# Performance work log

Hardware: AMD Instinct MI355X
Metric: run time of the kernel (lower is better)

Reference implementation:

```python
import jax, jax.numpy as jnp
import numpy as np

B, S, D = 1, 4096, 2048
M = 4                  # compression rate
NC = S // M            # compressed slots
TOPK = 512
NH, C = 16, 64         # query heads, head dim
DC = 512               # query compression dim
NG, DG = 4, 512        # output projection groups, intermediate dim
CI, NHI = 64, 4        # indexer head dim, indexer heads
ROPE = 32              # partial rope dims (last ROPE of C)
EPS = 1e-6
NEG = -1e30


def _ln(x, w, b):
    mu = x.mean(-1, keepdims=True)
    var = ((x - mu) ** 2).mean(-1, keepdims=True)
    return (x - mu) * jax.lax.rsqrt(var + EPS) * w + b


def _rope(q, pos):
    # partial RoPE on the last ROPE dims of q [B,S,NH,C]; keys are NOT rotated (faithful)
    x_part, x_rope = q[..., :C - ROPE], q[..., C - ROPE:]
    x0, x1 = x_rope[..., 0::2], x_rope[..., 1::2]
    inv = 1.0 / (10000.0 ** (jnp.arange(0, ROPE, 2, dtype=jnp.float32) / ROPE))
    ang = pos[:, None].astype(jnp.float32) * inv[None]           # [S, ROPE/2]
    cos = jnp.cos(ang)[None, :, None, :]
    sin = jnp.sin(ang)[None, :, None, :]
    r = x0 * cos - x1 * sin
    i = x0 * sin + x1 * cos
    rot = jnp.stack([r, i], -1).reshape(x_rope.shape)
    return jnp.concatenate([x_part, rot], -1)


def reference(x, w_kv_a, w_kv_b, w_z_a, w_z_b, b_a, b_b, w_dq, w_iuq, w_w, w_k,
              w_uq, o_down, o_up, kvn_w, kvn_b, qn_w, qn_b, sink_logits):
    pos = jnp.arange(S)
    # ---- token-level compressor: windowed (2m-wide, m-stride) per-channel softmax ----
    c_a = (x @ w_kv_a).reshape(B, NC, M, C)
    c_b = (x @ w_kv_b).reshape(B, NC, M, C)
    z_a = (x @ w_z_a).reshape(B, NC, M, C)
    z_b = (x @ w_z_b).reshape(B, NC, M, C)
    prev_z = jnp.concatenate([jnp.full((B, 1, M, C), NEG, x.dtype), z_b[:, :-1]], 1)
    prev_c = jnp.concatenate([jnp.zeros((B, 1, M, C), x.dtype), c_b[:, :-1]], 1)
    logits = jnp.concatenate([prev_z + b_b, z_a + b_a], 2)        # [B,NC,2M,C]
    wts = jax.nn.softmax(logits, axis=2)
    compressed = (wts * jnp.concatenate([prev_c, c_a], 2)).sum(2)  # [B,NC,C]
    # ---- lightning indexer: relu multi-head scores + causal mask + top-k ----
    c_q = x @ w_dq                                                 # [B,S,DC]
    q_i = (c_q @ w_iuq).reshape(B, S, NHI, CI)
    hw = x @ w_w                                                   # [B,S,NHI]
    k_orig = x.reshape(B, NC, M, D).mean(2)
    k_proj = k_orig @ w_k                                          # [B,NC,CI]
    dot = jnp.einsum('bshc,bkc->bskh', q_i, k_proj)
    iscores = (jax.nn.relu(dot) * hw[:, :, None, :]).sum(-1)       # [B,S,NC]
    imask = jnp.arange(NC)[None, None, :] < pos[None, :, None]     # NC//S + 1 == 1
    iscores = jnp.where(imask, iscores, -jnp.inf)
    _, top_idx = jax.lax.top_k(iscores, TOPK)                      # [B,S,K]
    # ---- sparse attention over gathered compressed KV ----
    q = (c_q @ w_uq).reshape(B, S, NH, C)
    kc = _ln(compressed, kvn_w, kvn_b)
    q = _rope(_ln(q, qn_w, qn_b), pos)
    k_sel = kc[jnp.arange(B)[:, None, None], top_idx]              # [B,S,K,C]
    scores = jnp.einsum('bshc,bskc->bhsk', q, k_sel) / jnp.sqrt(jnp.float32(C))
    cmask = pos[None, None, :, None] < (top_idx[:, None, :, :] * M)
    scores = jnp.where(cmask, scores, -jnp.inf)
    e = jnp.exp(scores)
    denom = e.sum(-1, keepdims=True) + jnp.exp(sink_logits)[None, :, None, None]
    attn = e / denom                                               # sink-augmented softmax
    out = jnp.einsum('bhsk,bskc->bshc', attn, k_sel).reshape(B, S, NH * C)
    g = jnp.einsum('bsgd,gde->bsge', out.reshape(B, S, NG, (NH * C) // NG), o_down)
    return g.reshape(B, S, NG * DG) @ o_up


def setup_inputs() -> dict:
    key = jax.random.key(0)
    ks = jax.random.split(key, 20)
    lin = lambda k, fi, fo: jax.random.normal(k, (fi, fo), jnp.float32) / np.sqrt(fi)
    return {
        'x': jax.random.normal(ks[0], (B, S, D), jnp.float32),
        'w_kv_a': lin(ks[1], D, C), 'w_kv_b': lin(ks[2], D, C),
        'w_z_a': lin(ks[3], D, C), 'w_z_b': lin(ks[4], D, C),
        'b_a': 0.02 * jax.random.normal(ks[5], (M, C), jnp.float32),
        'b_b': 0.02 * jax.random.normal(ks[6], (M, C), jnp.float32),
        'w_dq': lin(ks[7], D, DC),
        'w_iuq': lin(ks[8], DC, CI * NHI),
        'w_w': lin(ks[9], D, NHI),
        'w_k': lin(ks[10], D, CI),
        'w_uq': lin(ks[11], DC, NH * C),
        'o_down': jax.random.normal(ks[12], (NG, (NH * C) // NG, DG), jnp.float32) / np.sqrt((NH * C) // NG),
        'o_up': lin(ks[13], NG * DG, D),
        'kvn_w': 1.0 + 0.02 * jax.random.normal(ks[14], (C,), jnp.float32),
        'kvn_b': 0.02 * jax.random.normal(ks[15], (C,), jnp.float32),
        'qn_w': 1.0 + 0.02 * jax.random.normal(ks[16], (C,), jnp.float32),
        'qn_b': 0.02 * jax.random.normal(ks[17], (C,), jnp.float32),
        'sink_logits': 0.02 * jax.random.normal(ks[18], (NH,), jnp.float32),
    }
```

## Files before the change

### kernel.cpp

```cpp
#include <hip/hip_runtime.h>
#include <math.h>

#define S_   4096
#define D_   2048
#define M_   4
#define NC_  1024
#define TOPK_ 512
#define NH_  16
#define C_   64
#define DC_  512
#define NG_  4
#define DG_  512
#define CI_  64
#define NHI_ 4
#define ROPE_ 32
#define EPS_ 1e-6f

typedef __attribute__((ext_vector_type(8))) short short8;
typedef __attribute__((ext_vector_type(4))) short short4v;
typedef __attribute__((ext_vector_type(4))) float floatx4;

__device__ inline unsigned short f2bf(float f) {
  unsigned u = __float_as_uint(f);
  u += 0x7fff + ((u >> 16) & 1);
// ... 390 lines not shown
  float4 a = *(const float4*)&P[i];
  for (int s = 1; s < z; ++s) {
    float4 b = *(const float4*)&P[(size_t)s * n + i];
    a.x += b.x; a.y += b.y; a.z += b.z; a.w += b.w;
  }
  *(float4*)&C[i] = a;
}

__global__ void reduce_cast_split(const float* __restrict__ P, unsigned short* __restrict__ hi,
                                  unsigned short* __restrict__ lo, int n, int z) {
  int i = (blockIdx.x * 256 + threadIdx.x) * 4;
  if (i >= n) return;
  float4 a = *(const float4*)&P[i];
  for (int s = 1; s < z; ++s) {
    float4 b = *(const float4*)&P[(size_t)s * n + i];
    a.x += b.x; a.y += b.y; a.z += b.z; a.w += b.w;
  }
  ushort4 h = make_ushort4(f2bf(a.x), f2bf(a.y), f2bf(a.z), f2bf(a.w));
  ushort4 l = make_ushort4(f2bf(a.x - bf2f(h.x)), f2bf(a.y - bf2f(h.y)),
                           f2bf(a.z - bf2f(h.z)), f2bf(a.w - bf2f(h.w)));
  *(ushort4*)&hi[i] = h;
  *(ushort4*)&lo[i] = l;
}

__global__ __launch_bounds__(256) void iscores_mfma(
    const unsigned short* __restrict__ Ah, const unsigned short* __restrict__ Al,
    const unsigned short* __restrict__ Bh, const unsigned short* __restrict__ Bl,
    const float* __restrict__ hw, float* __restrict__ isc) {
  int bm = blockIdx.y * 128, bn = blockIdx.x * 128;
  if (bn > (bm >> 2) + 30) return;
  __shared__ unsigned short Ash[128 * 32];
  __shared__ unsigned short Asl[128 * 32];
  __shared__ unsigned short Bsh[128 * 32];
  __shared__ unsigned short Bsl[128 * 32];
  int tid = threadIdx.x;
  int lane = tid & 63, wid = tid >> 6;
  int wm = (wid >> 1) * 64, wn = (wid & 1) * 64;
  int qd = lane >> 4, m16 = lane & 15;

  floatx4 acc[4][4];
#pragma unroll
  for (int i = 0; i < 4; ++i)
#pragma unroll
    for (int j = 0; j < 4; ++j) acc[i][j] = (floatx4){0.f, 0.f, 0.f, 0.f};

#pragma unroll
  for (int k0 = 0; k0 < 64; k0 += 32) {
#pragma unroll
    for (int i = 0; i < 2; ++i) {
      int idx = tid + 256 * i;
      int r = idx >> 2, s = idx & 3;
      int g = s ^ ((r >> 1) & 3);
      size_t aoff = (size_t)(bm + r) * 64 + k0 + g * 8;
      size_t boff = (size_t)(bn + r) * 64 + k0 + g * 8;
      GLD16(Ah + aoff, &Ash[idx * 8]);
      GLD16(Al + aoff, &Asl[idx * 8]);
      GLD16(Bh + boff, &Bsh[idx * 8]);
      GLD16(Bl + boff, &Bsl[idx * 8]);
    }
    __syncthreads();
    short8 afh[4], afl[4], bfh[4], bfl[4];
#pragma unroll
    for (int mi = 0; mi < 4; ++mi) {
      int r = wm + mi * 16 + m16;
      int slot = qd ^ ((r >> 1) & 3);
      afh[mi] = *(const short8*)&Ash[r * 32 + slot * 8];
      afl[mi] = *(const short8*)&Asl[r * 32 + slot * 8];
    }
#pragma unroll
    for (int ni = 0; ni < 4; ++ni) {
      int r = wn + ni * 16 + m16;
      int slot = qd ^ ((r >> 1) & 3);
      bfh[ni] = *(const short8*)&Bsh[r * 32 + slot * 8];
      bfl[ni] = *(const short8*)&Bsl[r * 32 + slot * 8];
    }
#pragma unroll
    for (int mi = 0; mi < 4; ++mi)
#pragma unroll
      for (int ni = 0; ni < 4; ++ni) {
        acc[mi][ni] = __builtin_amdgcn_mfma_f32_16x16x32_bf16(afh[mi], bfh[ni], acc[mi][ni], 0, 0, 0);
        acc[mi][ni] = __builtin_amdgcn_mfma_f32_16x16x32_bf16(afh[mi], bfl[ni], acc[mi][ni], 0, 0, 0);
        acc[mi][ni] = __builtin_amdgcn_mfma_f32_16x16x32_bf16(afl[mi], bfh[ni], acc[mi][ni], 0, 0, 0);
      }
    __syncthreads();
  }
#pragma unroll
  for (int mi = 0; mi < 4; ++mi) {
    int tok = ((bm + wm + mi * 16) >> 2) + qd;
    float4 hwv = *(const float4*)&hw[tok * 4];
#pragma unroll
    for (int ni = 0; ni < 4; ++ni) {
      floatx4 a = acc[mi][ni];
      float v = fmaxf(a[0], 0.f) * hwv.x + fmaxf(a[1], 0.f) * hwv.y +
                fmaxf(a[2], 0.f) * hwv.z + fmaxf(a[3], 0.f) * hwv.w;
      int col = bn + wn + ni * 16 + m16;
      isc[(size_t)tok * NC_ + col] = (col < tok) ? v : -__builtin_inff();
    }
  }
}

#define BM 64
#define BN 64
#define BK 16
#define KSL_ 16
#define KSLICE_ 128
__global__ __launch_bounds__(256) void gemm_f32_splitk(
    const float* __restrict__ A, const float* __restrict__ B,
    float* __restrict__ P, int lda, int ldb) {
  __shared__ float As[BK][BM + 4];
  __shared__ float Bs[BK][BN + 4];
  int tid = threadIdx.x;
  int bm = blockIdx.y * BM;
  int kbase = blockIdx.x * KSLICE_;
  int tr = tid >> 4;
  int tc = tid & 15;
  float acc[4][4] = {{0.f}};
  for (int k0 = kbase; k0 < kbase + KSLICE_; k0 += BK) {
    int ac = tid & 15;
    int ar0 = tid >> 4;
#pragma unroll
    for (int i = 0; i < 4; ++i) {
      int r = ar0 + 16 * i;
      As[ac][r] = A[(size_t)(bm + r) * lda + k0 + ac];
    }
    int bc = tid & 63;
    int br0 = tid >> 6;
#pragma unroll
    for (int i = 0; i < 4; ++i) {
      int r = br0 + 4 * i;
      Bs[r][bc] = B[(size_t)(k0 + r) * ldb + bc];
    }
    __syncthreads();
#pragma unroll
    for (int kk = 0; kk < BK; ++kk) {
      float4 av = *(const float4*)&As[kk][tr * 4];
      float4 bv = *(const float4*)&Bs[kk][tc * 4];
      float a[4] = {av.x, av.y, av.z, av.w};
      float b[4] = {bv.x, bv.y, bv.z, bv.w};
#pragma unroll
      for (int i = 0; i < 4; ++i)
#pragma unroll
        for (int j = 0; j < 4; ++j) acc[i][j] += a[i] * b[j];
    }
    __syncthreads();
  }
  float* Pb = P + (size_t)blockIdx.x * (NC_ * CI_);
#pragma unroll
  for (int i = 0; i < 4; ++i) {
    float4 v = make_float4(acc[i][0], acc[i][1], acc[i][2], acc[i][3]);
    *(float4*)&Pb[(size_t)(bm + tr * 4 + i) * CI_ + tc * 4] = v;
  }
}

__global__ void reduce_splitk(const float* __restrict__ P, float* __restrict__ C) {
  int i = blockIdx.x * 256 + threadIdx.x;
  if (i >= NC_ * CI_) return;
  float a = 0.f;
#pragma unroll
  for (int s = 0; s < KSL_; ++s) a += P[(size_t)s * (NC_ * CI_) + i];
  C[i] = a;
}

__global__ void cast_bf16(const float* __restrict__ in, unsigned short* __restrict__ out, int n) {
  int i = (blockIdx.x * 256 + threadIdx.x) * 4;
  if (i >= n) return;
  float4 v = *(const float4*)&in[i];
  ushort4 o = make_ushort4(f2bf(v.x), f2bf(v.y), f2bf(v.z), f2bf(v.w));
  *(ushort4*)&out[i] = o;
}

__global__ void cast_split(const float* __restrict__ in, unsigned short* __restrict__ hi,
                           unsigned short* __restrict__ lo, int n) {
  int i = (blockIdx.x * 256 + threadIdx.x) * 4;
  if (i >= n) return;
  float4 v = *(const float4*)&in[i];
  ushort4 h = make_ushort4(f2bf(v.x), f2bf(v.y), f2bf(v.z), f2bf(v.w));
  ushort4 l = make_ushort4(f2bf(v.x - bf2f(h.x)), f2bf(v.y - bf2f(h.y)),
                           f2bf(v.z - bf2f(h.z)), f2bf(v.w - bf2f(h.w)));
  *(ushort4*)&hi[i] = h;
  *(ushort4*)&lo[i] = l;
}

__device__ inline float wave_sum64(float v) {
#pragma unroll
  for (int off = 32; off > 0; off >>= 1) v += __shfl_xor(v, off, 64);
  return v;
}

__global__ __launch_bounds__(512) void cast_split_hw_mean(
    const float* __restrict__ x, unsigned short* __restrict__ hi,
    unsigned short* __restrict__ lo, const float* __restrict__ ww,
    float* __restrict__ hw, float* __restrict__ ko) {
  int j = blockIdx.x, tid = threadIdx.x;
  int d0 = tid * 4;
  const float* wr = ww + d0 * 4;
  float4 v[4];
  float a[4][4];
#pragma unroll
  for (int m = 0; m < 4; ++m) {
    size_t i = (size_t)(j * 4 + m) * D_ + d0;
    v[m] = *(const float4*)&x[i];
    ushort4 h = make_ushort4(f2bf(v[m].x), f2bf(v[m].y), f2bf(v[m].z), f2bf(v[m].w));
    ushort4 l = make_ushort4(f2bf(v[m].x - bf2f(h.x)), f2bf(v[m].y - bf2f(h.y)),
                             f2bf(v[m].z - bf2f(h.z)), f2bf(v[m].w - bf2f(h.w)));
    *(ushort4*)&hi[i] = h;
    *(ushort4*)&lo[i] = l;
    a[m][0] = v[m].x * wr[0] + v[m].y * wr[4] + v[m].z * wr[8]  + v[m].w * wr[12];
    a[m][1] = v[m].x * wr[1] + v[m].y * wr[5] + v[m].z * wr[9]  + v[m].w * wr[13];
    a[m][2] = v[m].x * wr[2] + v[m].y * wr[6] + v[m].z * wr[10] + v[m].w * wr[14];
    a[m][3] = v[m].x * wr[3] + v[m].y * wr[7] + v[m].z * wr[11] + v[m].w * wr[15];
  }
  float4 s4;
  s4.x = 0.25f * (v[0].x + v[1].x + v[2].x + v[3].x);
  s4.y = 0.25f * (v[0].y + v[1].y + v[2].y + v[3].y);
  s4.z = 0.25f * (v[0].z + v[1].z + v[2].z + v[3].z);
  s4.w = 0.25f * (v[0].w + v[1].w + v[2].w + v[3].w);
  *(float4*)&ko[(size_t)j * D_ + d0] = s4;
#pragma unroll
  for (int m = 0; m < 4; ++m)
#pragma unroll
    for (int h2 = 0; h2 < 4; ++h2) a[m][h2] = wave_sum64(a[m][h2]);
  __shared__ float red[8][16];
  int wid = tid >> 6, lane = tid & 63;
  if (lane == 0) {
#pragma unroll
    for (int m = 0; m < 4; ++m)
#pragma unroll
      for (int h2 = 0; h2 < 4; ++h2) red[wid][m * 4 + h2] = a[m][h2];
  }
  __syncthreads();
  if (tid < 16) {
    float acc = 0.f;
#pragma unroll
    for (int w2 = 0; w2 < 8; ++w2) acc += red[w2][tid];
    hw[(size_t)(j * 4 + (tid >> 2)) * 4 + (tid & 3)] = acc;
  }
}

__global__ __launch_bounds__(256) void transpose_cast(
    const float* __restrict__ in, unsigned short* __restrict__ out, int K, int N,
    long long inz, long long outz) {
  in += (size_t)blockIdx.z * inz;
  out += (size_t)blockIdx.z * outz;
  __shared__ float t[32][33];
  int k0 = blockIdx.x * 32, n0 = blockIdx.y * 32;
  int tx = threadIdx.x & 31, ty = threadIdx.x >> 5;
#pragma unroll
  for (int i = 0; i < 4; ++i)
    t[ty * 4 + i][tx] = in[(size_t)(k0 + ty * 4 + i) * N + n0 + tx];
  __syncthreads();
#pragma unroll
  for (int i = 0; i < 4; ++i)
    out[(size_t)(n0 + ty * 4 + i) * K + k0 + tx] = f2bf(t[tx][ty * 4 + i]);
}

__global__ __launch_bounds__(256) void transpose_cast_split(
    const float* __restrict__ in, unsigned short* __restrict__ outh,
    unsigned short* __restrict__ outl, int K, int N) {
  __shared__ float t[32][33];
  int k0 = blockIdx.x * 32, n0 = blockIdx.y * 32;
  int tx = threadIdx.x & 31, ty = threadIdx.x >> 5;
#pragma unroll
  for (int i = 0; i < 4; ++i)
    t[ty * 4 + i][tx] = in[(size_t)(k0 + ty * 4 + i) * N + n0 + tx];
  __syncthreads();
#pragma unroll
  for (int i = 0; i < 4; ++i) {
    float v = t[tx][ty * 4 + i];
    unsigned short h = f2bf(v);
    outh[(size_t)(n0 + ty * 4 + i) * K + k0 + tx] = h;
    outl[(size_t)(n0 + ty * 4 + i) * K + k0 + tx] = f2bf(v - bf2f(h));
  }
}

__global__ void gate_kernel(const float* __restrict__ c4,
                            const float* __restrict__ ba, const float* __restrict__ bb,
                            float* __restrict__ comp) {
  int i = blockIdx.x * 256 + threadIdx.x;
  if (i >= NC_ * C_) return;
  int j = i >> 6, c = i & 63;
  float lg[8], vv[8];
#pragma unroll
  for (int m = 0; m < 4; ++m) {
    if (j == 0) {
      lg[m] = -1e30f + bb[m * C_ + c];
      vv[m] = 0.f;
    } else {
      int row = (j - 1) * 4 + m;
      lg[m] = c4[(size_t)row * 256 + 192 + c] + bb[m * C_ + c];
      vv[m] = c4[(size_t)row * 256 + 64 + c];
    }
    int row2 = j * 4 + m;
    lg[4 + m] = c4[(size_t)row2 * 256 + 128 + c] + ba[m * C_ + c];
    vv[4 + m] = c4[(size_t)row2 * 256 + 0 + c];
  }
  float mx = lg[0];
#pragma unroll
  for (int t = 1; t < 8; ++t) mx = fmaxf(mx, lg[t]);
  float se = 0.f, acc = 0.f;
#pragma unroll
  for (int t = 0; t < 8; ++t) {
    float e = expf(lg[t] - mx);
    se += e;
    acc += e * vv[t];
  }
  comp[i] = acc / se;
}

__global__ void ln_kc_kernel(const float* __restrict__ in, const float* __restrict__ w,
                             const float* __restrict__ b, unsigned short* __restrict__ kcb,
                             unsigned short* __restrict__ kcbT) {
  int row = blockIdx.x * 4 + (threadIdx.x >> 6);
  int c = threadIdx.x & 63;
  float v = in[(size_t)row * C_ + c];
  float mu = wave_sum64(v) * (1.f / 64.f);
  float d = v - mu;
  float var = wave_sum64(d * d) * (1.f / 64.f);
  float y = d * (1.f / sqrtf(var + EPS_)) * w[c] + b[c];
  unsigned short h = f2bf(y);
  kcb[(size_t)row * C_ + c] = h;
  kcbT[(size_t)c * NC_ + row] = h;
}

__global__ void rope_table_kernel(float* __restrict__ rt) {
  int i = blockIdx.x * 256 + threadIdx.x;
  if (i >= S_ * 16) return;
  int s = i >> 4, p = i & 15;
  float inv = powf(10000.f, -(2.f * (float)p) / (float)ROPE_);
  float ang = (float)s * inv;
  rt[i * 2] = cosf(ang);
  rt[i * 2 + 1] = sinf(ang);
}

__global__ void ln_rope_q_kernel(const float* __restrict__ quq, const float* __restrict__ w,
                                 const float* __restrict__ b, const float* __restrict__ rt,
                                 unsigned short* __restrict__ qb) {
  int row = blockIdx.x * 4 + (threadIdx.x >> 6);
  int s = row >> 4;
  int c = threadIdx.x & 63;
  float v = quq[(size_t)row * C_ + c];
  float mu = wave_sum64(v) * (1.f / 64.f);
  float d = v - mu;
  float var = wave_sum64(d * d) * (1.f / 64.f);
  float y = d * (1.f / sqrtf(var + EPS_)) * w[c] + b[c];
  float outv;
  float partner = __shfl_xor(y, 1, 64);
  if (c < C_ - ROPE_) {
    outv = y;
  } else {
    int p = (c - (C_ - ROPE_)) >> 1;
    float cs = rt[(s * 16 + p) * 2];
    float sn = rt[(s * 16 + p) * 2 + 1];
    if ((c & 1) == 0)
      outv = y * cs - partner * sn;
    else
      outv = partner * sn + y * cs;
  }
  qb[(size_t)row * C_ + c] = f2bf(outv * 0.125f);
}

#define MINF_ 0x007FFFFFu
__global__ __launch_bounds__(256) void topk_select_kernel(
    const float* __restrict__ isc, unsigned* __restrict__ sel) {
  __shared__ unsigned mv[NC_];
  __shared__ unsigned bins[256];
  __shared__ unsigned wsum[4];
  __shared__ unsigned sB, sR;
  __shared__ unsigned selw[32];
  int s = blockIdx.x;
  int tid = threadIdx.x;
  int w = tid >> 6, lane = tid & 63;
  if (tid < 32) selw[tid] = 0u;
  for (int i = tid; i < NC_; i += 256) {
    if (i < s) {
      unsigned u = __float_as_uint(isc[(size_t)s * NC_ + i]);
      mv[i] = (u & 0x80000000u) ? ~u : (u | 0x80000000u);
    } else {
      mv[i] = MINF_;
    }
  }
  __syncthreads();
  unsigned K_rem = TOPK_;
  unsigned prefix = 0u;
  for (int lvl = 0; lvl < 4; ++lvl) {
    int shift = 24 - 8 * lvl;
    unsigned pm = (lvl == 0) ? 0u : (0xFFFFFFFFu << (32 - 8 * lvl));
    bins[tid] = 0u;
    __syncthreads();
    for (int i = tid; i < NC_; i += 256) {
      unsigned m = mv[i];
      if ((m & pm) == prefix) atomicAdd(&bins[(m >> shift) & 0xFFu], 1u);
    }
    __syncthreads();
    unsigned v = bins[tid];
    unsigned p = v;
#pragma unroll
    for (int off = 1; off < 64; off <<= 1) {
      unsigned n = __shfl_up(p, (unsigned)off, 64);
      if (lane >= off) p += n;
    }
    if (lane == 63) wsum[w] = p;
    __syncthreads();
    unsigned T = 0, woff = 0;
#pragma unroll
    for (int i = 0; i < 4; ++i) {
      unsigned x_ = wsum[i];
      T += x_;
      if (i < w) woff += x_;
    }
    p += woff;
    unsigned gt = T - p;
    if (gt < K_rem && K_rem <= gt + v) { sB = (unsigned)tid; sR = K_rem - gt; }
    __syncthreads();
    prefix |= (sB << shift);
    K_rem = sR;
  }
  unsigned vstar = prefix;
  unsigned eq = 0;
#pragma unroll
  for (int j = 0; j < 4; ++j) eq += (mv[4 * tid + j] == vstar);
  unsigned rp = eq;
#pragma unroll
  for (int off = 1; off < 64; off <<= 1) {
    unsigned n = __shfl_up(rp, (unsigned)off, 64);
    if (lane >= off) rp += n;
  }
  if (lane == 63) wsum[w] = rp;
  __syncthreads();
  unsigned woff2 = 0;
#pragma unroll
  for (int i = 0; i < 4; ++i)
    if (i < w) woff2 += wsum[i];
  unsigned rank0 = rp + woff2 - eq;
  unsigned local = 0, bits = 0;
#pragma unroll
  for (int j = 0; j < 4; ++j) {
    unsigned m = mv[4 * tid + j];
    bool sb = (m > vstar) || (m == vstar && (rank0 + local) < K_rem);
    local += (m == vstar);
    if (sb) bits |= (1u << ((4 * tid + j) & 31));
  }
  if (bits) atomicOr(&selw[tid >> 3], bits);
  __syncthreads();
  if (tid < 32) sel[(size_t)s * 32 + tid] = selw[tid];
}

#define TS_ 8
__global__ __launch_bounds__(256) void attn_mfma_kernel(
    const unsigned short* __restrict__ qb, const unsigned short* __restrict__ kcb,
    const unsigned short* __restrict__ kcbT, const unsigned* __restrict__ sel,
    const float* __restrict__ sink, unsigned short* __restrict__ out) {
  __shared__ unsigned short p_s[128 * 72];
  __shared__ unsigned selw[TS_][32];
  int tid = threadIdx.x;
  int s0 = blockIdx.x * TS_;
  int lane = tid & 63, w = tid >> 6;
  int qd = lane >> 4, m16 = lane & 15;

  selw[tid >> 5][tid & 31] = sel[(size_t)(s0 + (tid >> 5)) * 32 + (tid & 31)];

  short8 qf[2][2];
#pragma unroll
  for (int tk = 0; tk < 2; ++tk)
#pragma unroll
    for (int ks = 0; ks < 2; ++ks)
      qf[tk][ks] = *(const short8*)&qb[(size_t)(s0 + 2 * w + tk) * 1024 + m16 * 64 + ks * 32 + qd * 8];

  floatx4 of[2][4];
#pragma unroll
  for (int i = 0; i < 2; ++i)
#pragma unroll
    for (int j = 0; j < 4; ++j) of[i][j] = (floatx4){0.f, 0.f, 0.f, 0.f};
  float dsum[2] = {0.f, 0.f};

  int ub = max(511, s0 + TS_ - 2);
  int ct_start = max(0, (s0 + 4) >> 8);
  int ct_end = min(16, (ub >> 6) + 1);

  for (int ct = ct_start; ct < ct_end; ++ct) {
    int c0 = ct * 64;
#pragma unroll
    for (int mc = 0; mc < 4; ++mc) {
      short8 a0 = *(const short8*)&kcb[(size_t)(c0 + mc * 16 + m16) * 64 + qd * 8];
      short8 a1 = *(const short8*)&kcb[(size_t)(c0 + mc * 16 + m16) * 64 + 32 + qd * 8];
#pragma unroll
      for (int nt = 0; nt < 2; ++nt) {
        floatx4 sc = (floatx4){0.f, 0.f, 0.f, 0.f};
        sc = __builtin_amdgcn_mfma_f32_16x16x32_bf16(a0, qf[nt][0], sc, 0, 0, 0);
        sc = __builtin_amdgcn_mfma_f32_16x16x32_bf16(a1, qf[nt][1], sc, 0, 0, 0);
        int tokL = 2 * w + nt;
        int sG = s0 + tokL;
        short4v pv;
#pragma unroll
        for (int rg = 0; rg < 4; ++rg) {
          int cG = c0 + mc * 16 + qd * 4 + rg;
          bool ok = (((selw[tokL][cG >> 5] >> (cG & 31)) & 1u) != 0u) && (sG < cG * 4);
          float e = ok ? __expf(sc[rg]) : 0.f;
          dsum[nt] += e;
          pv[rg] = (short)f2bf(e);
        }
        *(short4v*)&p_s[(tokL * 16 + m16) * 72 + mc * 16 + qd * 4] = pv;
      }
    }
#pragma unroll
    for (int ks = 0; ks < 2; ++ks) {
      short8 pa0 = *(const short8*)&p_s[((2 * w + 0) * 16 + m16) * 72 + ks * 32 + qd * 8];
      short8 pa1 = *(const short8*)&p_s[((2 * w + 1) * 16 + m16) * 72 + ks * 32 + qd * 8];
#pragma unroll
      for (int nt = 0; nt < 4; ++nt) {
        short8 bv = *(const short8*)&kcbT[(size_t)(nt * 16 + m16) * NC_ + c0 + ks * 32 + qd * 8];
        of[0][nt] = __builtin_amdgcn_mfma_f32_16x16x32_bf16(pa0, bv, of[0][nt], 0, 0, 0);
        of[1][nt] = __builtin_amdgcn_mfma_f32_16x16x32_bf16(pa1, bv, of[1][nt], 0, 0, 0);
      }
    }
  }
#pragma unroll
  for (int nt = 0; nt < 2; ++nt) {
    dsum[nt] += __shfl_xor(dsum[nt], 16, 64);
    dsum[nt] += __shfl_xor(dsum[nt], 32, 64);
  }
#pragma unroll
  for (int tk = 0; tk < 2; ++tk)
#pragma unroll
    for (int nt = 0; nt < 4; ++nt) {
      floatx4 o = of[tk][nt];
#pragma unroll
      for (int rg = 0; rg < 4; ++rg) {
        int head = qd * 4 + rg;
        float dn = __shfl(dsum[tk], head, 64) + __expf(sink[head]);
        out[(size_t)(s0 + 2 * w + tk) * 1024 + head * 64 + nt * 16 + m16] = f2bf(o[rg] / dn);
      }
    }
}

#define OFF_QUQ    0u
#define OFF_Q      4194304u
#define OFF_XH     8388608u
#define OFF_XL     12582912u
#define OFF_PART   16777216u
#define OFF_KO     18874368u
#define OFF_C4     20971520u
#define OFF_CQF    22020096u
#define OFF_RT     23134208u
#define OFF_WTB    24117248u
#define OFF_CQH    25165824u
#define OFF_CQL    26214400u
#define OFF_WPACKT 27262976u
#define OFF_WDQTH  27525120u
#define OFF_WDQTL  28049408u
#define OFF_WIUQTH 28573696u
#define OFF_WIUQTL 28639232u
#define OFF_WUQT   28704768u
#define OFF_ODB    28966912u
#define OFF_OUPT   29229056u
#define OFF_HW     31326208u
#define OFF_COMP   31342592u
#define OFF_KC     31408128u
#define OFF_KPR    31473664u

extern "C" void kernel_launch(void* const* d_in, const int* in_sizes, int n_in,
                              void* d_out, int out_size, void* d_ws, size_t ws_size,
                              hipStream_t stream) {
  const float* x      = (const float*)d_in[0];
  const float* w_kv_a = (const float*)d_in[1];
  const float* w_kv_b = (const float*)d_in[2];
  const float* w_z_a  = (const float*)d_in[3];
  const float* w_z_b  = (const float*)d_in[4];
  const float* b_a    = (const float*)d_in[5];
  const float* b_b    = (const float*)d_in[6];
  const float* w_dq   = (const float*)d_in[7];
  const float* w_iuq  = (const float*)d_in[8];
  const float* w_w    = (const float*)d_in[9];
  const float* w_k    = (const float*)d_in[10];
  const float* w_uq   = (const float*)d_in[11];
  const float* o_down = (const float*)d_in[12];
  const float* o_up   = (const float*)d_in[13];
  const float* kvn_w  = (const float*)d_in[14];
  const float* kvn_b  = (const float*)d_in[15];
  const float* qn_w   = (const float*)d_in[16];
  const float* qn_b   = (const float*)d_in[17];
  const float* sink   = (const float*)d_in[18];
  float* out = (float*)d_out;
  float* ws = (float*)d_ws;

  float* quq   = ws + OFF_QUQ;
  float* isc   = ws + OFF_QUQ;
  unsigned short* qb = (unsigned short*)(ws + OFF_Q);
  unsigned short* xh = (unsigned short*)(ws + OFF_XH);
  unsigned short* xl = (unsigned short*)(ws + OFF_XL);
  unsigned* sel = (unsigned*)(ws + OFF_XL);
  float* part  = ws + OFF_PART;
  float* k_or  = ws + OFF_KO;
  unsigned short* attnb = (unsigned short*)(ws + OFF_KO);
  float* c4    = ws + OFF_C4;
  unsigned short* qih = (unsigned short*)(ws + OFF_CQF);
  unsigned short* qil = qih + S_ * NHI_ * CI_;
  unsigned short* kph = qil + S_ * NHI_ * CI_;
  unsigned short* kpl = kph + NC_ * CI_;
  float* rt    = ws + OFF_RT;
  unsigned short* wtb = (unsigned short*)(ws + OFF_WTB);
  unsigned short* cqh = (unsigned short*)(ws + OFF_CQH);
  unsigned short* cql = (unsigned short*)(ws + OFF_CQL);
  unsigned short* wpackT = (unsigned short*)(ws + OFF_WPACKT);
  unsigned short* wdqTh  = (unsigned short*)(ws + OFF_WDQTH);
  unsigned short* wdqTl  = (unsigned short*)(ws + OFF_WDQTL);
  unsigned short* wiuqTh = (unsigned short*)(ws + OFF_WIUQTH);
  unsigned short* wiuqTl = (unsigned short*)(ws + OFF_WIUQTL);
  unsigned short* wuqT   = (unsigned short*)(ws + OFF_WUQT);
  unsigned short* odb    = (unsigned short*)(ws + OFF_ODB);
  unsigned short* oupT   = (unsigned short*)(ws + OFF_OUPT);
  float* hw    = ws + OFF_HW;
  float* comp  = ws + OFF_COMP;
  unsigned short* kcb  = (unsigned short*)(ws + OFF_KC);
  unsigned short* kcbT = kcb + NC_ * C_;
  float* k_pr  = ws + OFF_KPR;

  dim3 blk(256);

  cast_split_hw_mean<<<NC_, dim3(512), 0, stream>>>(x, xh, xl, w_w, hw, k_or);
  rope_table_kernel<<<256, blk, 0, stream>>>(rt);
  transpose_cast<<<dim3(64, 2), blk, 0, stream>>>(w_kv_a, wpackT + 0 * 64 * 2048, D_, C_, 0, 0);
  transpose_cast<<<dim3(64, 2), blk, 0, stream>>>(w_kv_b, wpackT + 1 * 64 * 2048, D_, C_, 0, 0);
  transpose_cast<<<dim3(64, 2), blk, 0, stream>>>(w_z_a,  wpackT + 2 * 64 * 2048, D_, C_, 0, 0);
  transpose_cast<<<dim3(64, 2), blk, 0, stream>>>(w_z_b,  wpackT + 3 * 64 * 2048, D_, C_, 0, 0);
  transpose_cast_split<<<dim3(64, 16), blk, 0, stream>>>(w_dq, wdqTh, wdqTl, D_, DC_);
  transpose_cast_split<<<dim3(16, 8), blk, 0, stream>>>(w_iuq, wiuqTh, wiuqTl, DC_, NHI_ * CI_);
  transpose_cast<<<dim3(16, 32), blk, 0, stream>>>(w_uq, wuqT, DC_, NH_ * C_, 0, 0);
  cast_bf16<<<512, blk, 0, stream>>>(o_down, odb, NG_ * 256 * DG_);
  transpose_cast<<<dim3(64, 64), blk, 0, stream>>>(o_up, oupT, NG_ * DG_, D_, 0, 0);

  gemm_bf16_64<<<dim3(2, 32, 4), blk, 0, stream>>>(
      oupT, odb, nullptr, wtb, DG_, D_, DG_, NG_ * 256,
      (long long)DG_, (long long)256 * DG_, 256LL);

  gemm_f32_splitk<<<dim3(KSL_, 16), blk, 0, stream>>>(k_or, w_k, part, D_, CI_);
  reduce_splitk<<<256, blk, 0, stream>>>(part, k_pr);

  gemm_bf16_split_128<<<dim3(4, 32, 4), blk, 0, stream>>>(xh, xl, wdqTh, wdqTl, ws,
                                                          512, D_, D_, DC_, 512, 512, (long long)S_ * DC_);
  reduce_cast_split<<<2048, blk, 0, stream>>>(ws, cqh, cql, S_ * DC_, 4);
  gemm_bf16_64<<<dim3(2, 64, 4), blk, 0, stream>>>(xh, wpackT, part, nullptr,
                                                   512, D_, D_, 256, 512, 512, (long long)S_ * 256);
  reduce_f32<<<1024, blk, 0, stream>>>(part, c4, S_ * 256, 4);
  gemm_bf16_split_64<<<dim3(2, 64, 4), blk, 0, stream>>>(cqh, cql, wiuqTh, wiuqTl, part,
                                                         128, DC_, DC_, 256, 128, 128, (long long)S_ * 256);
  reduce_cast_split<<<1024, blk, 0, stream>>>(part, qih, qil, S_ * 256, 4);
  gemm_bf16_64<<<dim3(8, 64, 1), blk, 0, stream>>>(cqh, wuqT, quq, nullptr,
                                                   DC_, DC_, DC_, NH_ * C_, 0, 0, 0);

  gate_kernel<<<256, blk, 0, stream>>>(c4, b_a, b_b, comp);
  ln_kc_kernel<<<256, blk, 0, stream>>>(comp, kvn_w, kvn_b, kcb, kcbT);

  ln_rope_q_kernel<<<16384, blk, 0, stream>>>(quq, qn_w, qn_b, rt, qb);

  cast_split<<<64, blk, 0, stream>>>(k_pr, kph, kpl, NC_ * CI_);
  iscores_mfma<<<dim3(8, 128), blk, 0, stream>>>(qih, qil, kph, kpl, hw, isc);
  topk_select_kernel<<<S_, blk, 0, stream>>>(isc, sel);

  attn_mfma_kernel<<<S_ / TS_, blk, 0, stream>>>(qb, kcb, kcbT, sel, sink, attnb);

  gemm_bf16_128<<<dim3(16, 32, 1), blk, 0, stream>>>(attnb, wtb, out, nullptr,
                                                     NG_ * 256, NH_ * C_, NG_ * 256, D_, 0, 0, 0);
}
```

Baseline: 410.9 us.

## Assign one query token per wave in sparse attention with 512-thread blocks

The attention kernel moves from 4 waves each handling 2 tokens to 8 waves each handling 1 token, using 512-thread blocks with the same 8 tokens per block. Selection bitmask words are now read straight from global memory per chunk, so the shared selw staging copy is gone, and the P scratch row stride shrinks from 72 to 68. This gives more waves to hide latency and fewer registers per thread. In exchange, each wave reloads the K tiles (kcb/kcbT) on its own, so less K data is reused within a wave.

```diff
diff --git a/kernel.cpp b/kernel.cpp
--- a/kernel.cpp
+++ b/kernel.cpp
@@ -860,91 +860,79 @@
 }
 
 #define TS_ 8
-__global__ __launch_bounds__(256) void attn_mfma_kernel(
+__global__ __launch_bounds__(512) void attn_mfma_kernel(
     const unsigned short* __restrict__ qb, const unsigned short* __restrict__ kcb,
     const unsigned short* __restrict__ kcbT, const unsigned* __restrict__ sel,
     const float* __restrict__ sink, unsigned short* __restrict__ out) {
-  __shared__ unsigned short p_s[128 * 72];
-  __shared__ unsigned selw[TS_][32];
+  __shared__ unsigned short p_s[128 * 68];
   int tid = threadIdx.x;
   int s0 = blockIdx.x * TS_;
   int lane = tid & 63, w = tid >> 6;
   int qd = lane >> 4, m16 = lane & 15;
-
-  selw[tid >> 5][tid & 31] = sel[(size_t)(s0 + (tid >> 5)) * 32 + (tid & 31)];
-
-  short8 qf[2][2];
-#pragma unroll
-  for (int tk = 0; tk < 2; ++tk)
-#pragma unroll
-    for (int ks = 0; ks < 2; ++ks)
-      qf[tk][ks] = *(const short8*)&qb[(size_t)(s0 + 2 * w + tk) * 1024 + m16 * 64 + ks * 32 + qd * 8];
-
-  floatx4 of[2][4];
-#pragma unroll
-  for (int i = 0; i < 2; ++i)
-#pragma unroll
-    for (int j = 0; j < 4; ++j) of[i][j] = (floatx4){0.f, 0.f, 0.f, 0.f};
-  float dsum[2] = {0.f, 0.f};
+  int sG = s0 + w;
+
+  short8 qf[2];
+#pragma unroll
+  for (int ks = 0; ks < 2; ++ks)
+    qf[ks] = *(const short8*)&qb[(size_t)sG * 1024 + m16 * 64 + ks * 32 + qd * 8];
+
+  floatx4 of[4];
+#pragma unroll
+  for (int j = 0; j < 4; ++j) of[j] = (floatx4){0.f, 0.f, 0.f, 0.f};
+  float dsum = 0.f;
 
   int ub = max(511, s0 + TS_ - 2);
   int ct_start = max(0, (s0 + 4) >> 8);
   int ct_end = min(16, (ub >> 6) + 1);
 
+  const unsigned* selrow = &sel[(size_t)sG * 32];
+
   for (int ct = ct_start; ct < ct_end; ++ct) {
     int c0 = ct * 64;
+    unsigned sw0 = selrow[ct * 2];
+    unsigned sw1 = selrow[ct * 2 + 1];
 #pragma unroll
     for (int mc = 0; mc < 4; ++mc) {
       short8 a0 = *(const short8*)&kcb[(size_t)(c0 + mc * 16 + m16) * 64 + qd * 8];
       short8 a1 = *(const short8*)&kcb[(size_t)(c0 + mc * 16 + m16) * 64 + 32 + qd * 8];
-#pragma unroll
-      for (int nt = 0; nt < 2; ++nt) {
-        floatx4 sc = (floatx4){0.f, 0.f, 0.f, 0.f};
-        sc = __builtin_amdgcn_mfma_f32_16x16x32_bf16(a0, qf[nt][0], sc, 0, 0, 0);
-        sc = __builtin_amdgcn_mfma_f32_16x16x32_bf16(a1, qf[nt][1], sc, 0, 0, 0);
-        int tokL = 2 * w + nt;
-        int sG = s0 + tokL;
-        short4v pv;
-#pragma unroll
-        for (int rg = 0; rg < 4; ++rg) {
-          int cG = c0 + mc * 16 + qd * 4 + rg;
-          bool ok = (((selw[tokL][cG >> 5] >> (cG & 31)) & 1u) != 0u) && (sG < cG * 4);
-          float e = ok ? __expf(sc[rg]) : 0.f;
-          dsum[nt] += e;
-          pv[rg] = (short)f2bf(e);
-        }
-        *(short4v*)&p_s[(tokL * 16 + m16) * 72 + mc * 16 + qd * 4] = pv;
-      }
+      floatx4 sc = (floatx4){0.f, 0.f, 0.f, 0.f};
+      sc = __builtin_amdgcn_mfma_f32_16x16x32_bf16(a0, qf[0], sc, 0, 0, 0);
+      sc = __builtin_amdgcn_mfma_f32_16x16x32_bf16(a1, qf[1], sc, 0, 0, 0);
+      unsigned sw = (mc < 2) ? sw0 : sw1;
+      short4v pv;
+#pragma unroll
+      for (int rg = 0; rg < 4; ++rg) {
+        int cG = c0 + mc * 16 + qd * 4 + rg;
+        int bitpos = (mc * 16 + qd * 4 + rg) & 31;
+        bool ok = (((sw >> bitpos) & 1u) != 0u) && (sG < cG * 4);
+        float e = ok ? __expf(sc[rg]) : 0.f;
+        dsum += e;
+        pv[rg] = (short)f2bf(e);
+      }
+      *(short4v*)&p_s[(w * 16 + m16) * 68 + mc * 16 + qd * 4] = pv;
     }
 #pragma unroll
     for (int ks = 0; ks < 2; ++ks) {
-      short8 pa0 = *(const short8*)&p_s[((2 * w + 0) * 16 + m16) * 72 + ks * 32 + qd * 8];
-      short8 pa1 = *(const short8*)&p_s[((2 * w + 1) * 16 + m16) * 72 + ks * 32 + qd * 8];
+      short8 pa = *(const short8*)&p_s[(w * 16 + m16) * 68 + ks * 32 + qd * 8];
 #pragma unroll
       for (int nt = 0; nt < 4; ++nt) {
         short8 bv = *(const short8*)&kcbT[(size_t)(nt * 16 + m16) * NC_ + c0 + ks * 32 + qd * 8];
-        of[0][nt] = __builtin_amdgcn_mfma_f32_16x16x32_bf16(pa0, bv, of[0][nt], 0, 0, 0);
-        of[1][nt] = __builtin_amdgcn_mfma_f32_16x16x32_bf16(pa1, bv, of[1][nt], 0, 0, 0);
-      }
-    }
-  }
-#pragma unroll
-  for (int nt = 0; nt < 2; ++nt) {
-    dsum[nt] += __shfl_xor(dsum[nt], 16, 64);
-    dsum[nt] += __shfl_xor(dsum[nt], 32, 64);
-  }
-#pragma unroll
-  for (int tk = 0; tk < 2; ++tk)
-#pragma unroll
-    for (int nt = 0; nt < 4; ++nt) {
-      floatx4 o = of[tk][nt];
-#pragma unroll
-      for (int rg = 0; rg < 4; ++rg) {
-        int head = qd * 4 + rg;
-        float dn = __shfl(dsum[tk], head, 64) + __expf(sink[head]);
-        out[(size_t)(s0 + 2 * w + tk) * 1024 + head * 64 + nt * 16 + m16] = f2bf(o[rg] / dn);
-      }
-    }
+        of[nt] = __builtin_amdgcn_mfma_f32_16x16x32_bf16(pa, bv, of[nt], 0, 0, 0);
+      }
+    }
+  }
+  dsum += __shfl_xor(dsum, 16, 64);
+  dsum += __shfl_xor(dsum, 32, 64);
+#pragma unroll
+  for (int nt = 0; nt < 4; ++nt) {
+    floatx4 o = of[nt];
+#pragma unroll
+    for (int rg = 0; rg < 4; ++rg) {
+      int head = qd * 4 + rg;
+      float dn = __shfl(dsum, head, 64) + __expf(sink[head]);
+      out[(size_t)sG * 1024 + head * 64 + nt * 16 + m16] = f2bf(o[rg] / dn);
+    }
+  }
 }
 
 #define OFF_QUQ    0u
@@ -1071,7 +1059,7 @@
   iscores_mfma<<<dim3(8, 128), blk, 0, stream>>>(qih, qil, kph, kpl, hw, isc);
   topk_select_kernel<<<S_, blk, 0, stream>>>(isc, sel);
 
-  attn_mfma_kernel<<<S_ / TS_, blk, 0, stream>>>(qb, kcb, kcbT, sel, sink, attnb);
+  attn_mfma_kernel<<<S_ / TS_, dim3(512), 0, stream>>>(qb, kcb, kcbT, sel, sink, attnb);
 
   gemm_bf16_128<<<dim3(16, 32, 1), blk, 0, stream>>>(attnb, wtb, out, nullptr,
                                                      NG_ * 256, NH_ * C_, NG_ * 256, D_, 0, 0, 0);
```

Measured after the change: 436.4 us. 1.06x slower.

## Fuse weight-prep, gate+LN, and split-K reduce+cast kernels; fold causal mask into top-k bits

Applied to the files above, without the earlier changes.

Ten separate weight transpose/cast launches plus the rope-table launch are merged into one prep kernel that dispatches on block index. The gate softmax is fused with the compressed-key layernorm, and the split-K reduction is fused with the hi/lo bf16 split cast. Together these remove several launches and intermediate buffers. The causal check moves from the attention inner loop into top-k bitmask construction, so attention reads a single preloaded selection word, and the P shared-memory row stride changes from 72 to 68. The stride change may alter LDS bank conflicts, and the mask move relies on top-k being the only producer of the selection bits.

```diff
diff --git a/kernel.cpp b/kernel.cpp
--- a/kernel.cpp
+++ b/kernel.cpp
@@ -566,33 +566,16 @@
   }
 }
 
-__global__ void reduce_splitk(const float* __restrict__ P, float* __restrict__ C) {
+__global__ void reduce_splitk_cast(const float* __restrict__ P,
+                                   unsigned short* __restrict__ hi,
+                                   unsigned short* __restrict__ lo) {
   int i = blockIdx.x * 256 + threadIdx.x;
-  if (i >= NC_ * CI_) return;
   float a = 0.f;
 #pragma unroll
   for (int s = 0; s < KSL_; ++s) a += P[(size_t)s * (NC_ * CI_) + i];
-  C[i] = a;
-}
-
-__global__ void cast_bf16(const float* __restrict__ in, unsigned short* __restrict__ out, int n) {
-  int i = (blockIdx.x * 256 + threadIdx.x) * 4;
-  if (i >= n) return;
-  float4 v = *(const float4*)&in[i];
-  ushort4 o = make_ushort4(f2bf(v.x), f2bf(v.y), f2bf(v.z), f2bf(v.w));
-  *(ushort4*)&out[i] = o;
-}
-
-__global__ void cast_split(const float* __restrict__ in, unsigned short* __restrict__ hi,
-                           unsigned short* __restrict__ lo, int n) {
-  int i = (blockIdx.x * 256 + threadIdx.x) * 4;
-  if (i >= n) return;
-  float4 v = *(const float4*)&in[i];
-  ushort4 h = make_ushort4(f2bf(v.x), f2bf(v.y), f2bf(v.z), f2bf(v.w));
-  ushort4 l = make_ushort4(f2bf(v.x - bf2f(h.x)), f2bf(v.y - bf2f(h.y)),
-                           f2bf(v.z - bf2f(h.z)), f2bf(v.w - bf2f(h.w)));
-  *(ushort4*)&hi[i] = h;
-  *(ushort4*)&lo[i] = l;
+  unsigned short h = f2bf(a);
+  hi[i] = h;
+  lo[i] = f2bf(a - bf2f(h));
 }
 
 __device__ inline float wave_sum64(float v) {
@@ -651,47 +634,108 @@
   }
 }
 
-__global__ __launch_bounds__(256) void transpose_cast(
-    const float* __restrict__ in, unsigned short* __restrict__ out, int K, int N,
-    long long inz, long long outz) {
-  in += (size_t)blockIdx.z * inz;
-  out += (size_t)blockIdx.z * outz;
+__global__ __launch_bounds__(256) void prep_kernel(
+    const float* __restrict__ w_kv_a, const float* __restrict__ w_kv_b,
+    const float* __restrict__ w_z_a, const float* __restrict__ w_z_b,
+    unsigned short* __restrict__ wpackT,
+    const float* __restrict__ w_dq, unsigned short* __restrict__ wdqTh,
+    unsigned short* __restrict__ wdqTl,
+    const float* __restrict__ w_iuq, unsigned short* __restrict__ wiuqTh,
+    unsigned short* __restrict__ wiuqTl,
+    const float* __restrict__ w_uq, unsigned short* __restrict__ wuqT,
+    const float* __restrict__ o_down, unsigned short* __restrict__ odb,
+    const float* __restrict__ o_up, unsigned short* __restrict__ oupT,
+    float* __restrict__ rt) {
   __shared__ float t[32][33];
-  int k0 = blockIdx.x * 32, n0 = blockIdx.y * 32;
-  int tx = threadIdx.x & 31, ty = threadIdx.x >> 5;
-#pragma unroll
-  for (int i = 0; i < 4; ++i)
-    t[ty * 4 + i][tx] = in[(size_t)(k0 + ty * 4 + i) * N + n0 + tx];
-  __syncthreads();
-#pragma unroll
-  for (int i = 0; i < 4; ++i)
-    out[(size_t)(n0 + ty * 4 + i) * K + k0 + tx] = f2bf(t[tx][ty * 4 + i]);
-}
-
-__global__ __launch_bounds__(256) void transpose_cast_split(
-    const float* __restrict__ in, unsigned short* __restrict__ outh,
-    unsigned short* __restrict__ outl, int K, int N) {
-  __shared__ float t[32][33];
-  int k0 = blockIdx.x * 32, n0 = blockIdx.y * 32;
-  int tx = threadIdx.x & 31, ty = threadIdx.x >> 5;
-#pragma unroll
-  for (int i = 0; i < 4; ++i)
-    t[ty * 4 + i][tx] = in[(size_t)(k0 + ty * 4 + i) * N + n0 + tx];
-  __syncthreads();
-#pragma unroll
-  for (int i = 0; i < 4; ++i) {
-    float v = t[tx][ty * 4 + i];
-    unsigned short h = f2bf(v);
-    outh[(size_t)(n0 + ty * 4 + i) * K + k0 + tx] = h;
-    outl[(size_t)(n0 + ty * 4 + i) * K + k0 + tx] = f2bf(v - bf2f(h));
-  }
-}
-
-__global__ void gate_kernel(const float* __restrict__ c4,
-                            const float* __restrict__ ba, const float* __restrict__ bb,
-                            float* __restrict__ comp) {
+  int b = blockIdx.x;
+  int tid = threadIdx.x;
+  int tx = tid & 31, ty = tid >> 5;
+  if (b < 512) {
+    int wsel = b >> 7, local = b & 127;
+    int bx = local & 63, by = local >> 6;
+    const float* in = (wsel == 0) ? w_kv_a : (wsel == 1) ? w_kv_b : (wsel == 2) ? w_z_a : w_z_b;
+    unsigned short* outp = wpackT + wsel * 64 * 2048;
+    int k0 = bx * 32, n0 = by * 32;
+#pragma unroll
+    for (int i = 0; i < 4; ++i)
+      t[ty * 4 + i][tx] = in[(size_t)(k0 + ty * 4 + i) * 64 + n0 + tx];
+    __syncthreads();
+#pragma unroll
+    for (int i = 0; i < 4; ++i)
+      outp[(size_t)(n0 + ty * 4 + i) * 2048 + k0 + tx] = f2bf(t[tx][ty * 4 + i]);
+  } else if (b < 1536) {
+    int local = b - 512;
+    int bx = local & 63, by = local >> 6;
+    int k0 = bx * 32, n0 = by * 32;
+#pragma unroll
+    for (int i = 0; i < 4; ++i)
+      t[ty * 4 + i][tx] = w_dq[(size_t)(k0 + ty * 4 + i) * 512 + n0 + tx];
+    __syncthreads();
+#pragma unroll
+    for (int i = 0; i < 4; ++i) {
+      float v = t[tx][ty * 4 + i];
+      unsigned short h = f2bf(v);
+      wdqTh[(size_t)(n0 + ty * 4 + i) * 2048 + k0 + tx] = h;
+      wdqTl[(size_t)(n0 + ty * 4 + i) * 2048 + k0 + tx] = f2bf(v - bf2f(h));
+    }
+  } else if (b < 1664) {
+    int local = b - 1536;
+    int bx = local & 15, by = local >> 4;
+    int k0 = bx * 32, n0 = by * 32;
+#pragma unroll
+    for (int i = 0; i < 4; ++i)
+      t[ty * 4 + i][tx] = w_iuq[(size_t)(k0 + ty * 4 + i) * 256 + n0 + tx];
+    __syncthreads();
+#pragma unroll
+    for (int i = 0; i < 4; ++i) {
+      float v = t[tx][ty * 4 + i];
+      unsigned short h = f2bf(v);
+      wiuqTh[(size_t)(n0 + ty * 4 + i) * 512 + k0 + tx] = h;
+      wiuqTl[(size_t)(n0 + ty * 4 + i) * 512 + k0 + tx] = f2bf(v - bf2f(h));
+    }
+  } else if (b < 2176) {
+    int local = b - 1664;
+    int bx = local & 15, by = local >> 4;
+    int k0 = bx * 32, n0 = by * 32;
+#pragma unroll
+    for (int i = 0; i < 4; ++i)
+      t[ty * 4 + i][tx] = w_uq[(size_t)(k0 + ty * 4 + i) * 1024 + n0 + tx];
+    __syncthreads();
+#pragma unroll
+    for (int i = 0; i < 4; ++i)
+      wuqT[(size_t)(n0 + ty * 4 + i) * 512 + k0 + tx] = f2bf(t[tx][ty * 4 + i]);
+  } else if (b < 2688) {
+    int i = ((b - 2176) * 256 + tid) * 4;
+    float4 v = *(const float4*)&o_down[i];
+    ushort4 o = make_ushort4(f2bf(v.x), f2bf(v.y), f2bf(v.z), f2bf(v.w));
+    *(ushort4*)&odb[i] = o;
+  } else if (b < 6784) {
+    int local = b - 2688;
+    int bx = local & 63, by = local >> 6;
+    int k0 = bx * 32, n0 = by * 32;
+#pragma unroll
+    for (int i = 0; i < 4; ++i)
+      t[ty * 4 + i][tx] = o_up[(size_t)(k0 + ty * 4 + i) * 2048 + n0 + tx];
+    __syncthreads();
+#pragma unroll
+    for (int i = 0; i < 4; ++i)
+      oupT[(size_t)(n0 + ty * 4 + i) * 2048 + k0 + tx] = f2bf(t[tx][ty * 4 + i]);
+  } else {
+    int i = (b - 6784) * 256 + tid;
+    int s = i >> 4, p = i & 15;
+    float inv = powf(10000.f, -(2.f * (float)p) / (float)ROPE_);
+    float ang = (float)s * inv;
+    rt[i * 2] = cosf(ang);
+    rt[i * 2 + 1] = sinf(ang);
+  }
+}
+
+__global__ void gate_ln_kernel(const float* __restrict__ c4,
+                               const float* __restrict__ ba, const float* __restrict__ bb,
+                               const float* __restrict__ w, const float* __restrict__ bias,
+                               unsigned short* __restrict__ kcb,
+                               unsigned short* __restrict__ kcbT) {
   int i = blockIdx.x * 256 + threadIdx.x;
-  if (i >= NC_ * C_) return;
   int j = i >> 6, c = i & 63;
   float lg[8], vv[8];
 #pragma unroll
@@ -718,32 +762,14 @@
     se += e;
     acc += e * vv[t];
   }
-  comp[i] = acc / se;
-}
-
-__global__ void ln_kc_kernel(const float* __restrict__ in, const float* __restrict__ w,
-                             const float* __restrict__ b, unsigned short* __restrict__ kcb,
-                             unsigned short* __restrict__ kcbT) {
-  int row = blockIdx.x * 4 + (threadIdx.x >> 6);
-  int c = threadIdx.x & 63;
-  float v = in[(size_t)row * C_ + c];
-  float mu = wave_sum64(v) * (1.f / 64.f);
-  float d = v - mu;
+  float cv = acc / se;
+  float mu = wave_sum64(cv) * (1.f / 64.f);
+  float d = cv - mu;
   float var = wave_sum64(d * d) * (1.f / 64.f);
-  float y = d * (1.f / sqrtf(var + EPS_)) * w[c] + b[c];
+  float y = d * (1.f / sqrtf(var + EPS_)) * w[c] + bias[c];
   unsigned short h = f2bf(y);
-  kcb[(size_t)row * C_ + c] = h;
-  kcbT[(size_t)c * NC_ + row] = h;
-}
-
-__global__ void rope_table_kernel(float* __restrict__ rt) {
-  int i = blockIdx.x * 256 + threadIdx.x;
-  if (i >= S_ * 16) return;
-  int s = i >> 4, p = i & 15;
-  float inv = powf(10000.f, -(2.f * (float)p) / (float)ROPE_);
-  float ang = (float)s * inv;
-  rt[i * 2] = cosf(ang);
-  rt[i * 2 + 1] = sinf(ang);
+  kcb[(size_t)j * C_ + c] = h;
+  kcbT[(size_t)c * NC_ + j] = h;
 }
 
 __global__ void ln_rope_q_kernel(const float* __restrict__ quq, const float* __restrict__ w,
@@ -850,9 +876,10 @@
 #pragma unroll
   for (int j = 0; j < 4; ++j) {
     unsigned m = mv[4 * tid + j];
-    bool sb = (m > vstar) || (m == vstar && (rank0 + local) < K_rem);
+    int idx = 4 * tid + j;
+    bool sb = ((m > vstar) || (m == vstar && (rank0 + local) < K_rem)) && (s < 4 * idx);
     local += (m == vstar);
-    if (sb) bits |= (1u << ((4 * tid + j) & 31));
+    if (sb) bits |= (1u << (idx & 31));
   }
   if (bits) atomicOr(&selw[tid >> 3], bits);
   __syncthreads();
@@ -864,7 +891,7 @@
     const unsigned short* __restrict__ qb, const unsigned short* __restrict__ kcb,
     const unsigned short* __restrict__ kcbT, const unsigned* __restrict__ sel,
     const float* __restrict__ sink, unsigned short* __restrict__ out) {
-  __shared__ unsigned short p_s[128 * 72];
+  __shared__ unsigned short p_s[128 * 68];
   __shared__ unsigned selw[TS_][32];
   int tid = threadIdx.x;
   int s0 = blockIdx.x * TS_;
@@ -903,23 +930,23 @@
         sc = __builtin_amdgcn_mfma_f32_16x16x32_bf16(a0, qf[nt][0], sc, 0, 0, 0);
         sc = __builtin_amdgcn_mfma_f32_16x16x32_bf16(a1, qf[nt][1], sc, 0, 0, 0);
         int tokL = 2 * w + nt;
-        int sG = s0 + tokL;
+        unsigned sw = selw[tokL][ct * 2 + (mc >> 1)];
         short4v pv;
 #pragma unroll
         for (int rg = 0; rg < 4; ++rg) {
-          int cG = c0 + mc * 16 + qd * 4 + rg;
-          bool ok = (((selw[tokL][cG >> 5] >> (cG & 31)) & 1u) != 0u) && (sG < cG * 4);
+          int bitpos = (mc * 16 + qd * 4 + rg) & 31;
+          bool ok = ((sw >> bitpos) & 1u) != 0u;
           float e = ok ? __expf(sc[rg]) : 0.f;
           dsum[nt] += e;
           pv[rg] = (short)f2bf(e);
         }
-        *(short4v*)&p_s[(tokL * 16 + m16) * 72 + mc * 16 + qd * 4] = pv;
+        *(short4v*)&p_s[(tokL * 16 + m16) * 68 + mc * 16 + qd * 4] = pv;
       }
     }
 #pragma unroll
     for (int ks = 0; ks < 2; ++ks) {
-      short8 pa0 = *(const short8*)&p_s[((2 * w + 0) * 16 + m16) * 72 + ks * 32 + qd * 8];
-      short8 pa1 = *(const short8*)&p_s[((2 * w + 1) * 16 + m16) * 72 + ks * 32 + qd * 8];
+      short8 pa0 = *(const short8*)&p_s[((2 * w + 0) * 16 + m16) * 68 + ks * 32 + qd * 8];
+      short8 pa1 = *(const short8*)&p_s[((2 * w + 1) * 16 + m16) * 68 + ks * 32 + qd * 8];
 #pragma unroll
       for (int nt = 0; nt < 4; ++nt) {
         short8 bv = *(const short8*)&kcbT[(size_t)(nt * 16 + m16) * NC_ + c0 + ks * 32 + qd * 8];
@@ -968,7 +995,6 @@
 #define OFF_ODB    28966912u
 #define OFF_OUPT   29229056u
 #define OFF_HW     31326208u
-#define OFF_COMP   31342592u
 #define OFF_KC     31408128u
 #define OFF_KPR    31473664u
 
@@ -1024,31 +1050,22 @@
   unsigned short* odb    = (unsigned short*)(ws + OFF_ODB);
   unsigned short* oupT   = (unsigned short*)(ws + OFF_OUPT);
   float* hw    = ws + OFF_HW;
-  float* comp  = ws + OFF_COMP;
   unsigned short* kcb  = (unsigned short*)(ws + OFF_KC);
   unsigned short* kcbT = kcb + NC_ * C_;
-  float* k_pr  = ws + OFF_KPR;
 
   dim3 blk(256);
 
   cast_split_hw_mean<<<NC_, dim3(512), 0, stream>>>(x, xh, xl, w_w, hw, k_or);
-  rope_table_kernel<<<256, blk, 0, stream>>>(rt);
-  transpose_cast<<<dim3(64, 2), blk, 0, stream>>>(w_kv_a, wpackT + 0 * 64 * 2048, D_, C_, 0, 0);
-  transpose_cast<<<dim3(64, 2), blk, 0, stream>>>(w_kv_b, wpackT + 1 * 64 * 2048, D_, C_, 0, 0);
-  transpose_cast<<<dim3(64, 2), blk, 0, stream>>>(w_z_a,  wpackT + 2 * 64 * 2048, D_, C_, 0, 0);
-  transpose_cast<<<dim3(64, 2), blk, 0, stream>>>(w_z_b,  wpackT + 3 * 64 * 2048, D_, C_, 0, 0);
-  transpose_cast_split<<<dim3(64, 16), blk, 0, stream>>>(w_dq, wdqTh, wdqTl, D_, DC_);
-  transpose_cast_split<<<dim3(16, 8), blk, 0, stream>>>(w_iuq, wiuqTh, wiuqTl, DC_, NHI_ * CI_);
-  transpose_cast<<<dim3(16, 32), blk, 0, stream>>>(w_uq, wuqT, DC_, NH_ * C_, 0, 0);
-  cast_bf16<<<512, blk, 0, stream>>>(o_down, odb, NG_ * 256 * DG_);
-  transpose_cast<<<dim3(64, 64), blk, 0, stream>>>(o_up, oupT, NG_ * DG_, D_, 0, 0);
+  prep_kernel<<<7040, blk, 0, stream>>>(w_kv_a, w_kv_b, w_z_a, w_z_b, wpackT,
+                                        w_dq, wdqTh, wdqTl, w_iuq, wiuqTh, wiuqTl,
+                                        w_uq, wuqT, o_down, odb, o_up, oupT, rt);
 
   gemm_bf16_64<<<dim3(2, 32, 4), blk, 0, stream>>>(
       oupT, odb, nullptr, wtb, DG_, D_, DG_, NG_ * 256,
       (long long)DG_, (long long)256 * DG_, 256LL);
 
   gemm_f32_splitk<<<dim3(KSL_, 16), blk, 0, stream>>>(k_or, w_k, part, D_, CI_);
-  reduce_splitk<<<256, blk, 0, stream>>>(part, k_pr);
+  reduce_splitk_cast<<<256, blk, 0, stream>>>(part, kph, kpl);
 
   gemm_bf16_split_128<<<dim3(4, 32, 4), blk, 0, stream>>>(xh, xl, wdqTh, wdqTl, ws,
                                                           512, D_, D_, DC_, 512, 512, (long long)S_ * DC_);
@@ -1062,12 +1079,10 @@
   gemm_bf16_64<<<dim3(8, 64, 1), blk, 0, stream>>>(cqh, wuqT, quq, nullptr,
                                                    DC_, DC_, DC_, NH_ * C_, 0, 0, 0);
 
-  gate_kernel<<<256, blk, 0, stream>>>(c4, b_a, b_b, comp);
-  ln_kc_kernel<<<256, blk, 0, stream>>>(comp, kvn_w, kvn_b, kcb, kcbT);
+  gate_ln_kernel<<<256, blk, 0, stream>>>(c4, b_a, b_b, kvn_w, kvn_b, kcb, kcbT);
 
   ln_rope_q_kernel<<<16384, blk, 0, stream>>>(quq, qn_w, qn_b, rt, qb);
 
-  cast_split<<<64, blk, 0, stream>>>(k_pr, kph, kpl, NC_ * CI_);
   iscores_mfma<<<dim3(8, 128), blk, 0, stream>>>(qih, qil, kph, kpl, hw, isc);
   topk_select_kernel<<<S_, blk, 0, stream>>>(isc, sel);
 
```

Result: faster. 390.5 us (-5.0%).
